# Kernel tuning notes

Hardware: AMD Instinct MI355X
Metric: run time of the kernel (lower is better)

## Reference

```python
import jax, jax.numpy as jnp
import numpy as np

HEADS = 16
CHUNK = 128  # chunked (mathematically exact) form of the causal cumsum linear attention
EPS = 0.001


def _linear_attention(q, k, v):
    # q, k, v: (B, H, L, d); q, k already SiLU-featurized
    B, H, L, d = q.shape
    Nc = L // CHUNK
    qc = q.reshape(B, H, Nc, CHUNK, d)
    kc = k.reshape(B, H, Nc, CHUNK, d)
    vc = v.reshape(B, H, Nc, CHUNK, d)

    # inter-chunk running state: S = cumsum of k (x) v over previous chunks, z = cumsum of k
    kv_chunk = jnp.einsum('bhncd,bhnce->bhnde', kc, vc)        # (B,H,Nc,d,d)
    S = jnp.cumsum(kv_chunk, axis=2) - kv_chunk                 # exclusive cumsum
    k_sum = kc.sum(axis=3)                                      # (B,H,Nc,d)
    z = jnp.cumsum(k_sum, axis=2) - k_sum                       # exclusive cumsum

    # intra-chunk causal part
    scores = jnp.einsum('bhnid,bhnjd->bhnij', qc, kc)           # (B,H,Nc,C,C)
    mask = jnp.tril(jnp.ones((CHUNK, CHUNK), dtype=bool))
    scores = jnp.where(mask, scores, jnp.zeros((), scores.dtype))
    num = jnp.einsum('bhnij,bhnje->bhnie', scores, vc)
    num = num + jnp.einsum('bhnid,bhnde->bhnie', qc, S)

    k_cum_local = jnp.cumsum(kc, axis=3)                        # within-chunk cumsum of k
    den = jnp.einsum('bhnid,bhnid->bhni', qc, k_cum_local)
    den = den + jnp.einsum('bhnid,bhnd->bhni', qc, z)

    out = num / jnp.maximum(den, EPS)[..., None]
    return out.reshape(B, H, L, d)


def setup_inputs() -> dict:
    key = jax.random.key(0)
    ks = jax.random.split(key, 9)
    D = 1024
    B, L = 4, 2048
    s = 0.02  # init scale
    return {
        'x':  jax.random.normal(ks[0], (B, L, D), dtype=jnp.float32),
        'Wq': jax.random.normal(ks[1], (D, D), dtype=jnp.float32) * s,
        'bq': jnp.zeros((D,), dtype=jnp.float32),
        'Wk': jax.random.normal(ks[2], (D, D), dtype=jnp.float32) * s,
        'bk': jnp.zeros((D,), dtype=jnp.float32),
        'Wv': jax.random.normal(ks[3], (D, D), dtype=jnp.float32) * s,
        'bv': jnp.zeros((D,), dtype=jnp.float32),
        'Wo': jax.random.normal(ks[4], (D, D), dtype=jnp.float32) * s,
        'bo': jnp.zeros((D,), dtype=jnp.float32),
    }


def reference(x, Wq, bq, Wk, bk, Wv, bv, Wo, bo):
    B, L, D = x.shape
    H = HEADS
    d = D // H
    # torch Linear: y = x @ W.T + b
    q = jax.nn.silu(x @ Wq.T + bq).reshape(B, L, H, d).transpose(0, 2, 1, 3)
    k = jax.nn.silu(x @ Wk.T + bk).reshape(B, L, H, d).transpose(0, 2, 1, 3)
    v = (x @ Wv.T + bv).reshape(B, L, H, d).transpose(0, 2, 1, 3)
    out = _linear_attention(q, k, v)                  # (B,H,L,d)
    out = out.transpose(0, 2, 1, 3).reshape(B, L, D)
    return out @ Wo.T + bo
```

## Files before the change

### kernel.cpp

```cpp
#include <hip/hip_runtime.h>
#include <math.h>

#define D_MODEL 1024
#define HEADS   16
#define HDIM    64
#define CHUNK   128
#define B_SZ    4
#define L_SEQ   2048
#define NCHUNK  16
#define NTOK    8192
#define EPS_DEN 1e-3f

typedef _Float16 half8 __attribute__((ext_vector_type(8)));
typedef _Float16 half4 __attribute__((ext_vector_type(4)));
typedef float    f32x4 __attribute__((ext_vector_type(4)));

__device__ __forceinline__ void gld_lds16(const void* g, void* l) {
    __builtin_amdgcn_global_load_lds(
        (const __attribute__((address_space(1))) void*)g,
        (__attribute__((address_space(3))) void*)l, 16, 0, 0);
}

__global__ __launch_bounds__(256) void prep(
    const float* __restrict__ x,  const float* __restrict__ Wq,
    const float* __restrict__ Wk, const float* __restrict__ Wv,
    const float* __restrict__ Wo, const float* __restrict__ bq,
    const float* __restrict__ bk,
    _Float16* __restrict__ x2,  _Float16* __restrict__ w2q,
    _Float16* __restrict__ w2k, _Float16* __restrict__ wv16,
    _Float16* __restrict__ wo16, float* __restrict__ bqk) {
    const int bid = blockIdx.x;
    if (bid < 5120) {
        const float* src; _Float16* dst; int t;
        if (bid < 4096)      { src = x;  dst = x2;  t = bid * 256 + threadIdx.x; }
        else if (bid < 4608) { src = Wq; dst = w2q; t = (bid - 4096) * 256 + threadIdx.x; }
        else                 { src = Wk; dst = w2k; t = (bid - 4608) * 256 + threadIdx.x; }
        int m = t >> 7, kc = (t & 127) << 3;
        const float* s = src + (size_t)m * 1024 + kc;
        f32x4 a = *(const f32x4*)s;
        f32x4 b = *(const f32x4*)(s + 4);
        float xs[8] = {a.x, a.y, a.z, a.w, b.x, b.y, b.z, b.w};
        half8 hi, lo;
        #pragma unroll
        for (int u = 0; u < 8; ++u) {
            _Float16 h = (_Float16)xs[u];
            hi[u] = h;
            lo[u] = (_Float16)(xs[u] - (float)h);
        }
        *(half8*)(dst + (size_t)m * 2048 + kc)        = hi;
        *(half8*)(dst + (size_t)m * 2048 + 1024 + kc) = lo;
    } else if (bid < 6144) {
        const float* src; _Float16* dst; int t;
        if (bid < 5632) { src = Wv; dst = wv16; t = (bid - 5120) * 256 + threadIdx.x; }
        else            { src = Wo; dst = wo16; t = (bid - 5632) * 256 + threadIdx.x; }
        int m = t >> 7, kc = (t & 127) << 3;
        const float* s = src + (size_t)m * 1024 + kc;
        f32x4 a = *(const f32x4*)s;
        f32x4 b = *(const f32x4*)(s + 4);
        float xs[8] = {a.x, a.y, a.z, a.w, b.x, b.y, b.z, b.w};
        half8 hv;
        #pragma unroll
        for (int u = 0; u < 8; ++u) hv[u] = (_Float16)xs[u];
        *(half8*)(dst + (size_t)m * 1024 + kc) = hv;
    } else {
        int i = (bid - 6144) * 256 + threadIdx.x;
        bqk[i] = (i < 1024) ? bq[i] : bk[i - 1024];
    }
}

__global__ __launch_bounds__(256, 4) void gemm_qkv(
    const _Float16* __restrict__ A,
    const _Float16* __restrict__ Bqk,
    const _Float16* __restrict__ Bv,
    const float* __restrict__ bqk, const float* __restrict__ bv,
    _Float16* __restrict__ Qlo, _Float16* __restrict__ Klo,
    _Float16* __restrict__ Q16, _Float16* __restrict__ K16,
    _Float16* __restrict__ V16, float* __restrict__ ksum) {
    __shared__ __align__(16) _Float16 sbuf[2 * 8192];
    __shared__ float sksum[2][128];
    _Float16* sC16 = sbuf;

    const int cb   = blockIdx.y;
    const int isqk = (cb < 16);
    const int isk  = (cb >= 8 && cb < 16);
    const int tid  = threadIdx.x;
    const int lane = tid & 63;
    const int w    = tid >> 6;
    const int row0 = blockIdx.x * 128;
    const int col0 = cb * 128;
    const int wm   = (w & 1) * 64;
    const int wn   = (w >> 1) * 64;

    const _Float16* B = isqk ? Bqk : Bv;
    const int ldb     = isqk ? 2048 : 1024;
    const int bcol0   = isqk ? col0 : col0 - 2048;
    const int kits    = isqk ? 96 : 32;

    const int ch0 = w * 64 + lane;
    const int rS0 = ch0 >> 2;
    const int cS0 = (ch0 & 3) ^ ((rS0 >> 1) & 3);
    const int ch1 = ch0 + 256;
    const int rS1 = ch1 >> 2;
    const int cS1 = (ch1 & 3) ^ ((rS1 >> 1) & 3);

    const _Float16* gA0 = A + (size_t)(row0  + rS0) * 2048 + cS0 * 8;
    const _Float16* gA1 = A + (size_t)(row0  + rS1) * 2048 + cS1 * 8;
    const _Float16* gB0 = B + (size_t)(bcol0 + rS0) * ldb  + cS0 * 8;
    const _Float16* gB1 = B + (size_t)(bcol0 + rS1) * ldb  + cS1 * 8;

    auto stage = [&](int kt, int bsel) {
        const int k0   = kt * 32;
        const int acol = (k0 < 2048) ? k0 : k0 - 2048;
        const int bcol = (k0 < 1024) ? k0 : k0 - 1024;
        _Float16* l = sbuf + bsel * 8192;
        gld_lds16(gA0 + acol, l + w * 512);
        gld_lds16(gA1 + acol, l + 2048 + w * 512);
        gld_lds16(gB0 + bcol, l + 4096 + w * 512);
        gld_lds16(gB1 + bcol, l + 6144 + w * 512);
    };

    f32x4 acc[4][4];
    #pragma unroll
    for (int i = 0; i < 4; ++i)
        #pragma unroll
        for (int j = 0; j < 4; ++j) { f32x4 z = {0.f, 0.f, 0.f, 0.f}; acc[i][j] = z; }

    const int ml = lane & 15;
    const int kg = lane >> 4;
    int offA[4], offB[4];
    #pragma unroll
    for (int i = 0; i < 4; ++i) {
        int r  = wm + i * 16 + ml;
        offA[i] = r * 32 + (kg ^ ((r >> 1) & 3)) * 8;
        int rn = wn + i * 16 + ml;
        offB[i] = 4096 + rn * 32 + (kg ^ ((rn >> 1) & 3)) * 8;
    }

    stage(0, 0);
    asm volatile("s_waitcnt vmcnt(0)\n\ts_barrier" ::: "memory");
    int cur = 0;
    for (int t = 0; t < kits; ++t) {
        if (t + 1 < kits) stage(t + 1, cur ^ 1);
        const _Float16* lb = sbuf + cur * 8192;
        half8 af[4], bf[4];
        #pragma unroll
        for (int i = 0; i < 4; ++i) {
            af[i] = *(const half8*)&lb[offA[i]];
            bf[i] = *(const half8*)&lb[offB[i]];
        }
        __builtin_amdgcn_s_setprio(1);
        #pragma unroll
        for (int i = 0; i < 4; ++i)
            #pragma unroll
            for (int j = 0; j < 4; ++j)
                acc[i][j] = __builtin_amdgcn_mfma_f32_16x16x32_f16(af[i], bf[j], acc[i][j], 0, 0, 0);
        __builtin_amdgcn_s_setprio(0);
        asm volatile("s_waitcnt vmcnt(0)\n\ts_barrier" ::: "memory");
        cur ^= 1;
    }

    const int colq = isqk ? ((col0 < 1024) ? col0 : col0 - 1024) : (col0 - 2048);
    _Float16* Ylo  = (col0 < 1024) ? Qlo : Klo;
    _Float16* Y16  = isqk ? ((col0 < 1024) ? Q16 : K16) : V16;

    const int rg = lane >> 4;
    #pragma unroll
    for (int j = 0; j < 4; ++j) {
        const float bvb = isqk ? bqk[col0 + wn + j * 16 + ml]
                               : bv[colq + wn + j * 16 + ml];
        const int nn = colq + wn + j * 16 + ml;
        #pragma unroll
        for (int i = 0; i < 4; ++i) {
            #pragma unroll
            for (int t = 0; t < 4; ++t) {
                float vv = acc[i][j][t] + bvb;
                if (isqk) {
                    vv = vv / (1.f + expf(-vv));
                    int mm = row0 + wm + i * 16 + rg * 4 + t;
                    _Float16 hv = (_Float16)vv;
                    Ylo[(size_t)mm * 1024 + nn] = (_Float16)(vv - (float)hv);
                }
                acc[i][j][t] = vv;
            }
        }
    }

    if (isk) {
        #pragma unroll
        for (int j = 0; j < 4; ++j) {
            float ps = 0.f;
            #pragma unroll
            for (int i = 0; i < 4; ++i)
                #pragma unroll
                for (int t = 0; t < 4; ++t) ps += acc[i][j][t];
            ps += __shfl_xor(ps, 16, 64);
            ps += __shfl_xor(ps, 32, 64);
            if (kg == 0) sksum[wm >> 6][wn + j * 16 + ml] = ps;
        }
        __syncthreads();
        if (tid < 128) {
            const int b = row0 >> 11;
            const int n = (row0 >> 7) & 15;
            const int cg = colq + tid;
            const int h = cg >> 6, f = cg & 63;
            ksum[(size_t)(((b * 16 + h) * 16 + n)) * 64 + f] =
                sksum[0][tid] + sksum[1][tid];
        }
        __syncthreads();
    }

    for (int s = 0; s < 4; ++s) {
        if ((wm == 0) == (s < 2)) {
            const int ib = (s & 1) * 2;
            #pragma unroll
            for (int ii = 0; ii < 2; ++ii)
                #pragma unroll
                for (int j = 0; j < 4; ++j)
                    #pragma unroll
                    for (int t = 0; t < 4; ++t) {
                        int lr = ii * 16 + rg * 4 + t;
                        sC16[lr * 136 + wn + j * 16 + ml] = (_Float16)acc[ib + ii][j][t];
                    }
        }
        __syncthreads();
        #pragma unroll
        for (int u = 0; u < 2; ++u) {
            int c = u * 256 + tid;
            int r = c >> 4, cc = (c & 15) * 8;
            half8 hv = *(const half8*)&sC16[r * 136 + cc];
            *(half8*)(Y16 + (size_t)(row0 + 32 * s + r) * 1024 + colq + cc) = hv;
        }
        __syncthreads();
    }
}

__global__ __launch_bounds__(256, 4) void gemm_out(
    const _Float16* __restrict__ A,
    const _Float16* __restrict__ B,
    const float* __restrict__ bias,
    float* __restrict__ Y) {
    __shared__ __align__(16) _Float16 sbuf[2 * 8192];

    const int tid  = threadIdx.x;
    const int lane = tid & 63;
    const int w    = tid >> 6;
    const int row0 = blockIdx.x * 128;
    const int col0 = blockIdx.y * 128;
    const int wm   = (w & 1) * 64;
    const int wn   = (w >> 1) * 64;

    const int ch0 = w * 64 + lane;
    const int rS0 = ch0 >> 2;
    const int cS0 = (ch0 & 3) ^ ((rS0 >> 1) & 3);
    const int ch1 = ch0 + 256;
    const int rS1 = ch1 >> 2;
    const int cS1 = (ch1 & 3) ^ ((rS1 >> 1) & 3);

    const _Float16* gA0 = A + (size_t)(row0 + rS0) * 1024 + cS0 * 8;
    const _Float16* gA1 = A + (size_t)(row0 + rS1) * 1024 + cS1 * 8;
    const _Float16* gB0 = B + (size_t)(col0 + rS0) * 1024 + cS0 * 8;
    const _Float16* gB1 = B + (size_t)(col0 + rS1) * 1024 + cS1 * 8;

    auto stage = [&](int kt, int bsel) {
        const int k0 = kt * 32;
        _Float16* l = sbuf + bsel * 8192;
        gld_lds16(gA0 + k0, l + w * 512);
        gld_lds16(gA1 + k0, l + 2048 + w * 512);
        gld_lds16(gB0 + k0, l + 4096 + w * 512);
        gld_lds16(gB1 + k0, l + 6144 + w * 512);
    };

    f32x4 acc[4][4];
    #pragma unroll
    for (int i = 0; i < 4; ++i)
        #pragma unroll
        for (int j = 0; j < 4; ++j) { f32x4 z = {0.f, 0.f, 0.f, 0.f}; acc[i][j] = z; }

    const int ml = lane & 15;
    const int kg = lane >> 4;
    int offA[4], offB[4];
    #pragma unroll
    for (int i = 0; i < 4; ++i) {
        int r  = wm + i * 16 + ml;
        offA[i] = r * 32 + (kg ^ ((r >> 1) & 3)) * 8;
        int rn = wn + i * 16 + ml;
        offB[i] = 4096 + rn * 32 + (kg ^ ((rn >> 1) & 3)) * 8;
    }

    stage(0, 0);
    asm volatile("s_waitcnt vmcnt(0)\n\ts_barrier" ::: "memory");
    int cur = 0;
    for (int kit = 0; kit < 32; ++kit) {
        if (kit + 1 < 32) stage(kit + 1, cur ^ 1);
        const _Float16* lb = sbuf + cur * 8192;
        half8 af[4], bf[4];
        #pragma unroll
        for (int i = 0; i < 4; ++i) {
            af[i] = *(const half8*)&lb[offA[i]];
            bf[i] = *(const half8*)&lb[offB[i]];
        }
        __builtin_amdgcn_s_setprio(1);
        #pragma unroll
        for (int i = 0; i < 4; ++i)
            #pragma unroll
            for (int j = 0; j < 4; ++j)
                acc[i][j] = __builtin_amdgcn_mfma_f32_16x16x32_f16(af[i], bf[j], acc[i][j], 0, 0, 0);
        __builtin_amdgcn_s_setprio(0);
        asm volatile("s_waitcnt vmcnt(0)\n\ts_barrier" ::: "memory");
        cur ^= 1;
    }

    const int rg = lane >> 4;
    #pragma unroll
    for (int j = 0; j < 4; ++j) {
        const int nn = col0 + wn + j * 16 + ml;
        const float bvb = bias[nn];
        #pragma unroll
        for (int i = 0; i < 4; ++i) {
            #pragma unroll
            for (int t = 0; t < 4; ++t) {
                int mm = row0 + wm + i * 16 + rg * 4 + t;
                Y[(size_t)mm * 1024 + nn] = acc[i][j][t] * 64.f + bvb;
            }
        }
    }
}

__global__ __launch_bounds__(256) void chunk_stats(
    const _Float16* __restrict__ k16g, const _Float16* __restrict__ v16g,
    float* __restrict__ kvT) {
    const int blk = blockIdx.x;
    const int n = blk & 15, bh = blk >> 4, h = bh & 15, b = bh >> 4;
    const size_t base = ((size_t)b * L_SEQ + (size_t)n * CHUNK) * D_MODEL + (size_t)h * HDIM;

    __shared__ __align__(16) _Float16 sv[64 * 136];
    __shared__ __align__(16) _Float16 sk[64 * 136];

    const int tid = threadIdx.x;
    #pragma unroll
    for (int p = 0; p < 4; ++p) {
        int idx = p * 256 + tid;
        int j = idx >> 3, c = idx & 7;
        half8 vv = *(const half8*)(v16g + base + (size_t)j * D_MODEL + c * 8);
        half8 kk = *(const half8*)(k16g + base + (size_t)j * D_MODEL + c * 8);
        #pragma unroll
        for (int u = 0; u < 8; ++u) {
            sv[(c * 8 + u) * 136 + j] = vv[u];
            sk[(c * 8 + u) * 136 + j] = kk[u];
        }
    }
    __syncthreads();

    const int lane = tid & 63;
    const int w    = tid >> 6;
    const int ml   = lane & 15;
    const int kg   = lane >> 4;

    f32x4 acc[4];
    #pragma unroll
    for (int ft = 0; ft < 4; ++ft) { f32x4 z = {0.f,0.f,0.f,0.f}; acc[ft] = z; }
    #pragma unroll
    for (int ft = 0; ft < 4; ++ft)
        #pragma unroll
        for (int kit = 0; kit < 4; ++kit) {
            half8 af = *(const half8*)&sv[(w * 16 + ml) * 136 + kit * 32 + kg * 8];
            half8 bf = *(const half8*)&sk[(ft * 16 + ml) * 136 + kit * 32 + kg * 8];
            acc[ft] = __builtin_amdgcn_mfma_f32_16x16x32_f16(af, bf, acc[ft], 0, 0, 0);
        }
    float* o = kvT + (size_t)blk * 4096;
    #pragma unroll
    for (int ft = 0; ft < 4; ++ft)
        #pragma unroll
        for (int t = 0; t < 4; ++t) {
            int e = w * 16 + kg * 4 + t;
            o[e * 64 + ft * 16 + ml] = acc[ft][t];
        }
}

__global__ __launch_bounds__(256) void scan_chunks(float* __restrict__ kvT,
                                                   float* __restrict__ ksum) {
    const int bh  = blockIdx.x >> 4;
    const int seg = blockIdx.x & 15;
    const int idx = seg * 256 + threadIdx.x;
    float* base = kvT + (size_t)bh * NCHUNK * 4096 + idx;
    float run = 0.f;
    #pragma unroll
    for (int nn = 0; nn < NCHUNK; ++nn) {
        float t = base[(size_t)nn * 4096];
        base[(size_t)nn * 4096] = run;
        run += t;
    }
    if (seg == 0 && threadIdx.x < 64) {
        float* zb = ksum + (size_t)bh * NCHUNK * 64 + threadIdx.x;
        float r2 = 0.f;
        #pragma unroll
        for (int nn = 0; nn < NCHUNK; ++nn) {
            float t = zb[nn * 64];
            zb[nn * 64] = r2;
            r2 += t;
        }
    }
}

__global__ __launch_bounds__(256) void attn_core(
    const _Float16* __restrict__ q16g, const _Float16* __restrict__ k16g,
    const _Float16* __restrict__ v16g, const _Float16* __restrict__ qlog,
    const _Float16* __restrict__ klog, const float* __restrict__ STg,
    const float* __restrict__ zg, _Float16* __restrict__ O16) {
    const int blk = blockIdx.x;
    const int n = blk & 15, bh = blk >> 4, h = bh & 15, b = bh >> 4;
    const size_t base = ((size_t)b * L_SEQ + (size_t)n * CHUNK) * D_MODEL + (size_t)h * HDIM;

    __shared__ __align__(16) _Float16 sq [128 * 72];
    __shared__ __align__(16) _Float16 sk [128 * 72];
    __shared__ __align__(16) _Float16 sv [64 * 136];
    __shared__ __align__(16) _Float16 sS [64 * 72];
    __shared__ __align__(16) _Float16 ssc[64 * 136];
    __shared__ float szz[64];

    const int tid = threadIdx.x;
    #pragma unroll
    for (int p = 0; p < 4; ++p) {
        int idx = p * 256 + tid;
        int j = idx >> 3, c = idx & 7;
        *(half8*)&sq[j * 72 + c * 8] = *(const half8*)(q16g + base + (size_t)j * D_MODEL + c * 8);
        *(half8*)&sk[j * 72 + c * 8] = *(const half8*)(k16g + base + (size_t)j * D_MODEL + c * 8);
        half8 vv = *(const half8*)(v16g + base + (size_t)j * D_MODEL + c * 8);
        #pragma unroll
        for (int u = 0; u < 8; ++u) sv[(c * 8 + u) * 136 + j] = vv[u];
    }
    #pragma unroll
    for (int p = 0; p < 2; ++p) {
        int idx = p * 256 + tid;
        int e = idx >> 3, c = idx & 7;
        f32x4 a = *(const f32x4*)(STg + (size_t)blk * 4096 + e * 64 + c * 8);
        f32x4 b4 = *(const f32x4*)(STg + (size_t)blk * 4096 + e * 64 + c * 8 + 4);
        half8 hv;
        hv[0] = (_Float16)a.x;  hv[1] = (_Float16)a.y;
        hv[2] = (_Float16)a.z;  hv[3] = (_Float16)a.w;
        hv[4] = (_Float16)b4.x; hv[5] = (_Float16)b4.y;
        hv[6] = (_Float16)b4.z; hv[7] = (_Float16)b4.w;
        *(half8*)&sS[e * 72 + c * 8] = hv;
    }
    if (tid < 64) szz[tid] = zg[(size_t)blk * 64 + tid];
    __syncthreads();

    const int lane = tid & 63;
    const int w    = tid >> 6;
    const int ml   = lane & 15;
    const int kg   = lane >> 4;

    for (int h2 = 0; h2 < 2; ++h2) {
        const int r0 = h2 * 64 + w * 16;
        const int rowmax = r0 + 15;

        half8 aflo[2];
        aflo[0] = *(const half8*)(qlog + base + (size_t)(r0 + ml) * D_MODEL + kg * 8);
        aflo[1] = *(const half8*)(qlog + base + (size_t)(r0 + ml) * D_MODEL + 32 + kg * 8);

        f32x4 acc1[8];
        #pragma unroll
        for (int nt = 0; nt < 8; ++nt) { f32x4 z = {0.f,0.f,0.f,0.f}; acc1[nt] = z; }
        #pragma unroll
        for (int nt = 0; nt < 8; ++nt) {
            if (nt * 16 <= rowmax) {
                #pragma unroll
                for (int kit = 0; kit < 2; ++kit) {
                    half8 af = *(const half8*)&sq[(r0 + ml) * 72 + kit * 32 + kg * 8];
                    half8 bf = *(const half8*)&sk[(nt * 16 + ml) * 72 + kit * 32 + kg * 8];
                    acc1[nt] = __builtin_amdgcn_mfma_f32_16x16x32_f16(af, bf, acc1[nt], 0, 0, 0);
                }
            }
        }
        #pragma unroll
        for (int nt = 0; nt < 8; ++nt) {
            if (nt * 16 <= rowmax) {
                const _Float16* kb = klog + base + (size_t)(nt * 16 + ml) * D_MODEL;
                half8 bl0 = *(const half8*)(kb + kg * 8);
                half8 bl1 = *(const half8*)(kb + 32 + kg * 8);
                half8 ah0 = *(const half8*)&sq[(r0 + ml) * 72 + kg * 8];
                half8 ah1 = *(const half8*)&sq[(r0 + ml) * 72 + 32 + kg * 8];
                half8 bh0 = *(const half8*)&sk[(nt * 16 + ml) * 72 + kg * 8];
                half8 bh1 = *(const half8*)&sk[(nt * 16 + ml) * 72 + 32 + kg * 8];
                acc1[nt] = __builtin_amdgcn_mfma_f32_16x16x32_f16(ah0, bl0, acc1[nt], 0, 0, 0);
                acc1[nt] = __builtin_amdgcn_mfma_f32_16x16x32_f16(ah1, bl1, acc1[nt], 0, 0, 0);
                acc1[nt] = __builtin_amdgcn_mfma_f32_16x16x32_f16(aflo[0], bh0, acc1[nt], 0, 0, 0);
                acc1[nt] = __builtin_amdgcn_mfma_f32_16x16x32_f16(aflo[1], bh1, acc1[nt], 0, 0, 0);
            }
        }

        float rs[4];
        #pragma unroll
        for (int t = 0; t < 4; ++t) {
            const int ig = r0 + kg * 4 + t;
            float s = 0.f;
            #pragma unroll
            for (int nt = 0; nt < 8; ++nt) {
                int jg = nt * 16 + ml;
                s += (jg <= ig) ? acc1[nt][t] : 0.f;
            }
            const int f0 = ml * 4;
            half4 ql = *(const half4*)(qlog + base + (size_t)ig * D_MODEL + f0);
            #pragma unroll
            for (int u = 0; u < 4; ++u)
                s += ((float)sq[ig * 72 + f0 + u] + (float)ql[u]) * szz[f0 + u];
            s += __shfl_xor(s, 1, 64);
            s += __shfl_xor(s, 2, 64);
            s += __shfl_xor(s, 4, 64);
            s += __shfl_xor(s, 8, 64);
            rs[t] = s;
        }

        #pragma unroll
        for (int nt = 0; nt < 8; ++nt) {
            #pragma unroll
            for (int t = 0; t < 4; ++t) {
                int lr = w * 16 + kg * 4 + t;
                int ig = h2 * 64 + lr;
                int jg = nt * 16 + ml;
                float val = (jg <= ig) ? acc1[nt][t] : 0.f;
                ssc[lr * 136 + jg] = (_Float16)val;
            }
        }
        __syncthreads();

        f32x4 acc2[4];
        #pragma unroll
        for (int et = 0; et < 4; ++et) { f32x4 z = {0.f,0.f,0.f,0.f}; acc2[et] = z; }
        const int nkit = (h2 == 0) ? 2 : 4;
        #pragma unroll
        for (int et = 0; et < 4; ++et) {
            for (int kit = 0; kit < nkit; ++kit) {
                half8 af = *(const half8*)&ssc[(w * 16 + ml) * 136 + kit * 32 + kg * 8];
                half8 bf = *(const half8*)&sv[(et * 16 + ml) * 136 + kit * 32 + kg * 8];
                acc2[et] = __builtin_amdgcn_mfma_f32_16x16x32_f16(af, bf, acc2[et], 0, 0, 0);
            }
            #pragma unroll
            for (int kit = 0; kit < 2; ++kit) {
                half8 af = *(const half8*)&sq[(r0 + ml) * 72 + kit * 32 + kg * 8];
                half8 bf = *(const half8*)&sS[(et * 16 + ml) * 72 + kit * 32 + kg * 8];
                acc2[et] = __builtin_amdgcn_mfma_f32_16x16x32_f16(af, bf, acc2[et], 0, 0, 0);
            }
        }
        #pragma unroll
        for (int t = 0; t < 4; ++t) {
            int lr = w * 16 + kg * 4 + t;
            int ig = h2 * 64 + lr;
            float rc = 0.015625f / fmaxf(rs[t], EPS_DEN);
            #pragma unroll
            for (int et = 0; et < 4; ++et) {
                int e = et * 16 + ml;
                O16[base + (size_t)ig * D_MODEL + e] = (_Float16)(acc2[et][t] * rc);
            }
        }
        __syncthreads();
    }
}

extern "C" void kernel_launch(void* const* d_in, const int* in_sizes, int n_in,
                              void* d_out, int out_size, void* d_ws, size_t ws_size,
                              hipStream_t stream) {
    const float* x  = (const float*)d_in[0];
    const float* Wq = (const float*)d_in[1];
    const float* bq = (const float*)d_in[2];
    const float* Wk = (const float*)d_in[3];
    const float* bk = (const float*)d_in[4];
    const float* Wv = (const float*)d_in[5];
    const float* bv = (const float*)d_in[6];
    const float* Wo = (const float*)d_in[7];
    const float* bo = (const float*)d_in[8];
    float* out = (float*)d_out;

    char* p = (char*)d_ws;
    _Float16* x2   = (_Float16*)p;  p += (size_t)NTOK * 2048 * 2;
    _Float16* w2q  = (_Float16*)p;  p += (size_t)1024 * 2048 * 2;
    _Float16* w2k  = (_Float16*)p;  p += (size_t)1024 * 2048 * 2;
    _Float16* wv16 = (_Float16*)p;  p += (size_t)1024 * 1024 * 2;
    _Float16* wo16 = (_Float16*)p;  p += (size_t)1024 * 1024 * 2;
    _Float16* qlo  = (_Float16*)p;  p += (size_t)NTOK * 1024 * 2;
    _Float16* klo  = (_Float16*)p;  p += (size_t)NTOK * 1024 * 2;
    _Float16* q16  = (_Float16*)p;  p += (size_t)NTOK * 1024 * 2;
    _Float16* k16  = (_Float16*)p;  p += (size_t)NTOK * 1024 * 2;
    _Float16* v16  = (_Float16*)p;  p += (size_t)NTOK * 1024 * 2;
    float* kvT  = (float*)p;        p += (size_t)1024 * 4096 * 4;
    float* ksb  = (float*)p;        p += (size_t)1024 * 64 * 4;
    float* bqk  = (float*)p;        p += 2048 * 4;
    _Float16* attn16 = x2;

    prep<<<6152, 256, 0, stream>>>(x, Wq, Wk, Wv, Wo, bq, bk,
                                   x2, w2q, w2k, wv16, wo16, bqk);

    gemm_qkv<<<dim3(64, 24), 256, 0, stream>>>(x2, w2q, wv16, bqk, bv,
                                               qlo, klo, q16, k16, v16, ksb);

    chunk_stats<<<1024, 256, 0, stream>>>(k16, v16, kvT);
    scan_chunks<<<1024, 256, 0, stream>>>(kvT, ksb);
    attn_core<<<1024, 256, 0, stream>>>(q16, k16, v16, qlo, klo, kvT, ksb, attn16);

    gemm_out<<<dim3(64, 8), 256, 0, stream>>>(attn16, wo16, bo, out);
}
```

Measured before the change: 338.6 us.

## Stage low-part k in swizzled LDS, emit fp16 prefix state, batch QK passes

The scan kernel writes the exclusive prefix state directly as fp16 into a new buffer, so attn_core no longer reads fp32 and converts it. attn_core loads the low-precision k residual once into swizzled shared memory, reusing the score buffer, instead of reloading it from global memory for every tile. Both 64-row QK accumulations now run before the finish phases so there is more independent MFMA work. This doubles the live accumulator registers, which may reduce occupancy.

```diff
diff --git a/kernel.cpp b/kernel.cpp
--- a/kernel.cpp
+++ b/kernel.cpp
@@ -377,17 +377,19 @@
         }
 }
 
-__global__ __launch_bounds__(256) void scan_chunks(float* __restrict__ kvT,
+__global__ __launch_bounds__(256) void scan_chunks(const float* __restrict__ kvT,
+                                                   _Float16* __restrict__ kv16,
                                                    float* __restrict__ ksum) {
     const int bh  = blockIdx.x >> 4;
     const int seg = blockIdx.x & 15;
     const int idx = seg * 256 + threadIdx.x;
-    float* base = kvT + (size_t)bh * NCHUNK * 4096 + idx;
+    const float* base = kvT + (size_t)bh * NCHUNK * 4096 + idx;
+    _Float16*   obase = kv16 + (size_t)bh * NCHUNK * 4096 + idx;
     float run = 0.f;
     #pragma unroll
     for (int nn = 0; nn < NCHUNK; ++nn) {
         float t = base[(size_t)nn * 4096];
-        base[(size_t)nn * 4096] = run;
+        obase[(size_t)nn * 4096] = (_Float16)run;
         run += t;
     }
     if (seg == 0 && threadIdx.x < 64) {
@@ -405,7 +407,7 @@
 __global__ __launch_bounds__(256) void attn_core(
     const _Float16* __restrict__ q16g, const _Float16* __restrict__ k16g,
     const _Float16* __restrict__ v16g, const _Float16* __restrict__ qlog,
-    const _Float16* __restrict__ klog, const float* __restrict__ STg,
+    const _Float16* __restrict__ klog, const _Float16* __restrict__ ST16,
     const float* __restrict__ zg, _Float16* __restrict__ O16) {
     const int blk = blockIdx.x;
     const int n = blk & 15, bh = blk >> 4, h = bh & 15, b = bh >> 4;
@@ -417,6 +419,7 @@
     __shared__ __align__(16) _Float16 sS [64 * 72];
     __shared__ __align__(16) _Float16 ssc[64 * 136];
     __shared__ float szz[64];
+    _Float16* sklo = ssc;
 
     const int tid = threadIdx.x;
     #pragma unroll
@@ -428,19 +431,15 @@
         half8 vv = *(const half8*)(v16g + base + (size_t)j * D_MODEL + c * 8);
         #pragma unroll
         for (int u = 0; u < 8; ++u) sv[(c * 8 + u) * 136 + j] = vv[u];
+        half8 kl = *(const half8*)(klog + base + (size_t)j * D_MODEL + c * 8);
+        *(half8*)&sklo[j * 64 + ((c ^ (j & 7)) << 3)] = kl;
     }
     #pragma unroll
     for (int p = 0; p < 2; ++p) {
         int idx = p * 256 + tid;
         int e = idx >> 3, c = idx & 7;
-        f32x4 a = *(const f32x4*)(STg + (size_t)blk * 4096 + e * 64 + c * 8);
-        f32x4 b4 = *(const f32x4*)(STg + (size_t)blk * 4096 + e * 64 + c * 8 + 4);
-        half8 hv;
-        hv[0] = (_Float16)a.x;  hv[1] = (_Float16)a.y;
-        hv[2] = (_Float16)a.z;  hv[3] = (_Float16)a.w;
-        hv[4] = (_Float16)b4.x; hv[5] = (_Float16)b4.y;
-        hv[6] = (_Float16)b4.z; hv[7] = (_Float16)b4.w;
-        *(half8*)&sS[e * 72 + c * 8] = hv;
+        *(half8*)&sS[e * 72 + c * 8] =
+            *(const half8*)(ST16 + (size_t)blk * 4096 + e * 64 + c * 8);
     }
     if (tid < 64) szz[tid] = zg[(size_t)blk * 64 + tid];
     __syncthreads();
@@ -450,17 +449,16 @@
     const int ml   = lane & 15;
     const int kg   = lane >> 4;
 
-    for (int h2 = 0; h2 < 2; ++h2) {
-        const int r0 = h2 * 64 + w * 16;
+    f32x4 acc1a[8], acc1b[8];
+    #pragma unroll
+    for (int nt = 0; nt < 8; ++nt) {
+        f32x4 z = {0.f,0.f,0.f,0.f}; acc1a[nt] = z; acc1b[nt] = z;
+    }
+
+    auto qk_acc = [&](f32x4 (&a1)[8], int r0) {
         const int rowmax = r0 + 15;
-
-        half8 aflo[2];
-        aflo[0] = *(const half8*)(qlog + base + (size_t)(r0 + ml) * D_MODEL + kg * 8);
-        aflo[1] = *(const half8*)(qlog + base + (size_t)(r0 + ml) * D_MODEL + 32 + kg * 8);
-
-        f32x4 acc1[8];
-        #pragma unroll
-        for (int nt = 0; nt < 8; ++nt) { f32x4 z = {0.f,0.f,0.f,0.f}; acc1[nt] = z; }
+        half8 aflo0 = *(const half8*)(qlog + base + (size_t)(r0 + ml) * D_MODEL + kg * 8);
+        half8 aflo1 = *(const half8*)(qlog + base + (size_t)(r0 + ml) * D_MODEL + 32 + kg * 8);
         #pragma unroll
         for (int nt = 0; nt < 8; ++nt) {
             if (nt * 16 <= rowmax) {
@@ -468,27 +466,33 @@
                 for (int kit = 0; kit < 2; ++kit) {
                     half8 af = *(const half8*)&sq[(r0 + ml) * 72 + kit * 32 + kg * 8];
                     half8 bf = *(const half8*)&sk[(nt * 16 + ml) * 72 + kit * 32 + kg * 8];
-                    acc1[nt] = __builtin_amdgcn_mfma_f32_16x16x32_f16(af, bf, acc1[nt], 0, 0, 0);
+                    a1[nt] = __builtin_amdgcn_mfma_f32_16x16x32_f16(af, bf, a1[nt], 0, 0, 0);
                 }
             }
         }
         #pragma unroll
         for (int nt = 0; nt < 8; ++nt) {
             if (nt * 16 <= rowmax) {
-                const _Float16* kb = klog + base + (size_t)(nt * 16 + ml) * D_MODEL;
-                half8 bl0 = *(const half8*)(kb + kg * 8);
-                half8 bl1 = *(const half8*)(kb + 32 + kg * 8);
+                const int jr = nt * 16 + ml;
+                half8 bl0 = *(const half8*)&sklo[jr * 64 + ((kg ^ (jr & 7)) << 3)];
+                half8 bl1 = *(const half8*)&sklo[jr * 64 + (((4 + kg) ^ (jr & 7)) << 3)];
                 half8 ah0 = *(const half8*)&sq[(r0 + ml) * 72 + kg * 8];
                 half8 ah1 = *(const half8*)&sq[(r0 + ml) * 72 + 32 + kg * 8];
-                half8 bh0 = *(const half8*)&sk[(nt * 16 + ml) * 72 + kg * 8];
-                half8 bh1 = *(const half8*)&sk[(nt * 16 + ml) * 72 + 32 + kg * 8];
-                acc1[nt] = __builtin_amdgcn_mfma_f32_16x16x32_f16(ah0, bl0, acc1[nt], 0, 0, 0);
-                acc1[nt] = __builtin_amdgcn_mfma_f32_16x16x32_f16(ah1, bl1, acc1[nt], 0, 0, 0);
-                acc1[nt] = __builtin_amdgcn_mfma_f32_16x16x32_f16(aflo[0], bh0, acc1[nt], 0, 0, 0);
-                acc1[nt] = __builtin_amdgcn_mfma_f32_16x16x32_f16(aflo[1], bh1, acc1[nt], 0, 0, 0);
-            }
-        }
-
+                half8 bh0 = *(const half8*)&sk[jr * 72 + kg * 8];
+                half8 bh1 = *(const half8*)&sk[jr * 72 + 32 + kg * 8];
+                a1[nt] = __builtin_amdgcn_mfma_f32_16x16x32_f16(ah0, bl0, a1[nt], 0, 0, 0);
+                a1[nt] = __builtin_amdgcn_mfma_f32_16x16x32_f16(ah1, bl1, a1[nt], 0, 0, 0);
+                a1[nt] = __builtin_amdgcn_mfma_f32_16x16x32_f16(aflo0, bh0, a1[nt], 0, 0, 0);
+                a1[nt] = __builtin_amdgcn_mfma_f32_16x16x32_f16(aflo1, bh1, a1[nt], 0, 0, 0);
+            }
+        }
+    };
+    qk_acc(acc1a, w * 16);
+    qk_acc(acc1b, 64 + w * 16);
+    __syncthreads();
+
+    auto finish = [&](f32x4 (&a1)[8], int h2, int nkit) {
+        const int r0 = h2 * 64 + w * 16;
         float rs[4];
         #pragma unroll
         for (int t = 0; t < 4; ++t) {
@@ -497,7 +501,7 @@
             #pragma unroll
             for (int nt = 0; nt < 8; ++nt) {
                 int jg = nt * 16 + ml;
-                s += (jg <= ig) ? acc1[nt][t] : 0.f;
+                s += (jg <= ig) ? a1[nt][t] : 0.f;
             }
             const int f0 = ml * 4;
             half4 ql = *(const half4*)(qlog + base + (size_t)ig * D_MODEL + f0);
@@ -518,7 +522,7 @@
                 int lr = w * 16 + kg * 4 + t;
                 int ig = h2 * 64 + lr;
                 int jg = nt * 16 + ml;
-                float val = (jg <= ig) ? acc1[nt][t] : 0.f;
+                float val = (jg <= ig) ? a1[nt][t] : 0.f;
                 ssc[lr * 136 + jg] = (_Float16)val;
             }
         }
@@ -527,7 +531,6 @@
         f32x4 acc2[4];
         #pragma unroll
         for (int et = 0; et < 4; ++et) { f32x4 z = {0.f,0.f,0.f,0.f}; acc2[et] = z; }
-        const int nkit = (h2 == 0) ? 2 : 4;
         #pragma unroll
         for (int et = 0; et < 4; ++et) {
             for (int kit = 0; kit < nkit; ++kit) {
@@ -554,7 +557,9 @@
             }
         }
         __syncthreads();
-    }
+    };
+    finish(acc1a, 0, 2);
+    finish(acc1b, 1, 4);
 }
 
 extern "C" void kernel_launch(void* const* d_in, const int* in_sizes, int n_in,
@@ -583,6 +588,7 @@
     _Float16* k16  = (_Float16*)p;  p += (size_t)NTOK * 1024 * 2;
     _Float16* v16  = (_Float16*)p;  p += (size_t)NTOK * 1024 * 2;
     float* kvT  = (float*)p;        p += (size_t)1024 * 4096 * 4;
+    _Float16* kv16 = (_Float16*)p;  p += (size_t)1024 * 4096 * 2;
     float* ksb  = (float*)p;        p += (size_t)1024 * 64 * 4;
     float* bqk  = (float*)p;        p += 2048 * 4;
     _Float16* attn16 = x2;
@@ -594,8 +600,8 @@
                                                qlo, klo, q16, k16, v16, ksb);
 
     chunk_stats<<<1024, 256, 0, stream>>>(k16, v16, kvT);
-    scan_chunks<<<1024, 256, 0, stream>>>(kvT, ksb);
-    attn_core<<<1024, 256, 0, stream>>>(q16, k16, v16, qlo, klo, kvT, ksb, attn16);
+    scan_chunks<<<1024, 256, 0, stream>>>(kvT, kv16, ksb);
+    attn_core<<<1024, 256, 0, stream>>>(q16, k16, v16, qlo, klo, kv16, ksb, attn16);
 
     gemm_out<<<dim3(64, 8), 256, 0, stream>>>(attn16, wo16, bo, out);
 }
```

After: 330.6 us. 2.4% less time.
